# Kernel optimization log

Measured on AMD Instinct MI355X. Metric: run time of the kernel, lower is better.

The kernel has to match this reference:

```python
import jax, jax.numpy as jnp
import numpy as np

N_QUBITS = 10


def _apply_1q(state, U, wire, n):
    # state: (B, 2**n) complex; apply 2x2 U on `wire` (wire 0 = most significant bit)
    B = state.shape[0]
    left = 2 ** wire
    right = 2 ** (n - wire - 1)
    s = state.reshape(B, left, 2, right)
    s = jnp.einsum('ij,bljr->blir', U, s)
    return s.reshape(B, 2 ** n)


def _cnot(state, c, t, n):
    # CNOT with control wire c, target wire t
    B = state.shape[0]
    s = state.reshape((B,) + (2,) * n)
    ci, ti = c + 1, t + 1
    flipped = jnp.flip(s, axis=ti)
    zero = jnp.take(s, 0, axis=ci)      # control=0 slice unchanged
    one = jnp.take(flipped, 1, axis=ci)  # control=1 slice with target flipped
    s = jnp.stack([zero, one], axis=ci)
    return s.reshape(B, 2 ** n)


def _rot_matrix(phi, theta, omega):
    # PennyLane Rot(phi, theta, omega) = RZ(omega) @ RY(theta) @ RZ(phi)
    c = jnp.cos(theta / 2).astype(jnp.complex64)
    s = jnp.sin(theta / 2).astype(jnp.complex64)
    ep = jnp.exp(-0.5j * (phi + omega).astype(jnp.complex64))  # e^{-i(phi+omega)/2}
    em = jnp.exp(0.5j * (phi - omega).astype(jnp.complex64))   # e^{ i(phi-omega)/2}
    row0 = jnp.stack([ep * c, -em * s])
    row1 = jnp.stack([jnp.conj(em) * s, jnp.conj(ep) * c])
    return jnp.stack([row0, row1])  # (2, 2)


def setup_inputs() -> dict:
    key = jax.random.key(0)
    k1, k2 = jax.random.split(key)
    B, dim = 8192, 2 ** N_QUBITS
    patch = jax.random.normal(k1, (B, dim), dtype=jnp.float32)
    patch = patch / jnp.linalg.norm(patch, axis=1, keepdims=True)  # L2-normalized amplitudes
    weights = 0.01 * jax.random.normal(k2, (N_QUBITS, 3), dtype=jnp.float32)
    return {"patch_batch": patch, "weights": weights}


def reference(patch_batch, weights):
    n = weights.shape[0]
    state = patch_batch.astype(jnp.complex64)  # amplitude embedding
    for w in range(n):
        U = _rot_matrix(weights[w, 0], weights[w, 1], weights[w, 2])
        state = _apply_1q(state, U, w, n)
    for w in range(n - 1):
        state = _cnot(state, w, w + 1, n)
    state = _cnot(state, n - 1, 0, n)
    # expectation values of X, Y, Z on wire 0
    s2 = state.reshape(-1, 2, 2 ** (n - 1))
    a0, a1 = s2[:, 0], s2[:, 1]
    z = jnp.sum(jnp.conj(a0) * a1, axis=1)
    ex = 2.0 * jnp.real(z)
    ey = 2.0 * jnp.imag(z)
    ez = jnp.sum(jnp.abs(a0) ** 2 - jnp.abs(a1) ** 2, axis=1)
    out = jnp.stack([ex, ey, ez], axis=1)  # (B, 3)
    return jnp.nan_to_num(out, nan=0.0, posinf=1.0, neginf=-1.0)
```

## Files before the change

kernel.cpp:

```cpp
#include <hip/hip_runtime.h>


__global__ void qk_setup(const float* __restrict__ w, float* __restrict__ ws) {
    int t = threadIdx.x;
    if (t < 10) {
        float th = w[3 * t + 1];
        ws[2 * t]     = cosf(0.5f * th);
        ws[2 * t + 1] = sinf(0.5f * th);
    }
    if (t < 16) {
        float a = 0.f;
        for (int j = 0; j < 4; j++) if ((t >> j) & 1) a += w[3 * (9 - j)];
        ws[32 + 2 * t]     = cosf(a);
        ws[32 + 2 * t + 1] = sinf(a);
    }
    {
        float a = 0.f;
        for (int j = 0; j < 6; j++) if ((t >> j) & 1) a += w[3 * (5 - j)];
        ws[64 + 2 * t]     = cosf(a);
        ws[64 + 2 * t + 1] = sinf(a);
    }
    if (t < 4) {
        float d = (1.f - 2.f * ((t >> 1) & 1)) * w[2] + (1.f - 2.f * (t & 1)) * w[5];
        ws[192 + 2 * t]     = cosf(d);
        ws[192 + 2 * t + 1] = sinf(d);
    }
}

__global__ __launch_bounds__(256) void qk_sim(const float* __restrict__ x,
                                              const float* __restrict__ ws,
                                              float* __restrict__ out,
                                              int nstates) {
    int wave = (int)((blockIdx.x * blockDim.x + threadIdx.x) >> 6);
    int lane = threadIdx.x & 63;
    if (wave >= nstates) return;

    const float* CS = ws;
    const float* R  = ws + 32;
    const float* L  = ws + 64;
    const float* T4 = ws + 192;

    float Lr = L[2 * lane], Li = L[2 * lane + 1];

    const float4* row = (const float4*)(x + (size_t)wave * 1024);
    float re[16], im[16];
#pragma unroll
    for (int k = 0; k < 4; k++) {
        float4 v = row[lane * 4 + k];
        float xs0 = v.x, xs1 = v.y, xs2 = v.z, xs3 = v.w;
        float xv[4] = {xs0, xs1, xs2, xs3};
#pragma unroll
        for (int j = 0; j < 4; j++) {
            int r = 4 * k + j;
            float ar = xv[j] * R[2 * r];
            float ai = xv[j] * R[2 * r + 1];
            re[r] = Lr * ar - Li * ai;
            im[r] = Lr * ai + Li * ar;
        }
    }

#pragma unroll
    for (int rb = 0; rb < 4; rb++) {
        float c = CS[2 * (9 - rb)], s = CS[2 * (9 - rb) + 1];
#pragma unroll
        for (int r0 = 0; r0 < 16; r0++) {
            if (r0 & (1 << rb)) continue;
            int r1 = r0 | (1 << rb);
            float a0r = re[r0], a0i = im[r0];
            float a1r = re[r1], a1i = im[r1];
            re[r0] = c * a0r - s * a1r;  im[r0] = c * a0i - s * a1i;
            re[r1] = s * a0r + c * a1r;  im[r1] = s * a0i + c * a1i;
        }
    }

#pragma unroll
    for (int l = 0; l < 6; l++) {
        float c = CS[2 * (5 - l)], s = CS[2 * (5 - l) + 1];
        float ss = ((lane >> l) & 1) ? s : -s;
#pragma unroll
        for (int r = 0; r < 16; r++) {
            float mr = re[r], mi = im[r];
            float pr = __shfl_xor(mr, 1 << l, 64);
            float pi = __shfl_xor(mi, 1 << l, 64);
            re[r] = c * mr + ss * pr;
            im[r] = c * mi + ss * pi;
        }
    }

    float zxr = 0.f, zxi = 0.f, zyr = 0.f, zyi = 0.f, ez = 0.f;
#pragma unroll
    for (int r = 0; r < 16; r++) {
        float mr = re[r], mi = im[r];
        float pr = __shfl_xor(mr, 48, 64);
        float pi = __shfl_xor(mi, 48, 64);
        float cr = mr * pr + mi * pi;
        float ci = mr * pi - mi * pr;
        zxr += cr; zxi += ci;
        if (__popc(r) & 1) { zyr -= cr; zyi -= ci; ez -= mr * mr + mi * mi; }
        else               { zyr += cr; zyi += ci; ez += mr * mr + mi * mi; }
    }
    int j4 = (lane >> 4) & 3;
    float cD = T4[2 * j4], sD = T4[2 * j4 + 1];
    float lsgn = (__popc(lane & 31) & 1) ? -1.f : 1.f;
    float ex  = cD * zxr - sD * zxi;
    float ey  = lsgn * (cD * zyi + sD * zyr);
    float ezl = lsgn * ez;

#pragma unroll
    for (int off = 32; off >= 1; off >>= 1) {
        ex  += __shfl_xor(ex,  off, 64);
        ey  += __shfl_xor(ey,  off, 64);
        ezl += __shfl_xor(ezl, off, 64);
    }
    if (lane == 0) {
        float* o = out + 3 * (size_t)wave;
        o[0] = ex; o[1] = ey; o[2] = ezl;
    }
}

extern "C" void kernel_launch(void* const* d_in, const int* in_sizes, int n_in,
                              void* d_out, int out_size, void* d_ws, size_t ws_size,
                              hipStream_t stream) {
    const float* patch   = (const float*)d_in[0];
    const float* weights = (const float*)d_in[1];
    float* out = (float*)d_out;
    float* ws  = (float*)d_ws;

    int nstates = in_sizes[0] / 1024;

    qk_setup<<<1, 64, 0, stream>>>(weights, ws);

    int nblocks = nstates / 4;
    qk_sim<<<nblocks, 256, 0, stream>>>(patch, ws, out, nstates);
}
```

Baseline: 93.89 us.

## Remap qubits to registers/lanes, precompute full phase table, use DPP cross-lane ops

Changes the assignment of amplitudes to lanes and registers so each lane loads strided float4 rows (h*64+lane). Precomputes a full 1024-entry complex phase table in the setup kernel instead of the separate L and R factors. Replaces ds_bpermute shuffles with DPP and ds_swizzle for the small xor distances, and computes the wire-0 pairing inside registers rather than via a cross-lane shuffle. This cuts shuffle traffic and per-element complex multiplies, at the cost of an extra 8 KB phase-table read per wave and a larger setup kernel.

```diff
diff --git a/kernel.cpp b/kernel.cpp
--- a/kernel.cpp
+++ b/kernel.cpp
@@ -1,29 +1,64 @@
 #include <hip/hip_runtime.h>
 
 
+template <int CTRL>
+__device__ __forceinline__ float dppf(float x) {
+    return __int_as_float(__builtin_amdgcn_update_dpp(
+        __float_as_int(x), __float_as_int(x), CTRL, 0xF, 0xF, true));
+}
+
+template <int MASK>
+__device__ __forceinline__ float lxor(float x) {
+    if constexpr (MASK == 1)  return dppf<0xB1>(x);
+    else if constexpr (MASK == 2)  return dppf<0x4E>(x);
+    else if constexpr (MASK == 4)  return dppf<0x141>(dppf<0x1B>(x));
+    else if constexpr (MASK == 8)  return dppf<0x128>(x);
+    else if constexpr (MASK == 16)
+        return __int_as_float(__builtin_amdgcn_ds_swizzle(__float_as_int(x), 0x401F));
+    else return __shfl_xor(x, MASK, 64);
+}
+
 __global__ void qk_setup(const float* __restrict__ w, float* __restrict__ ws) {
     int t = threadIdx.x;
+    float a = 0.f;
+    for (int wq = 0; wq < 10; wq++)
+        if ((t >> (9 - wq)) & 1) a += w[3 * wq];
+    ws[2 * t]     = cosf(a);
+    ws[2 * t + 1] = sinf(a);
     if (t < 10) {
         float th = w[3 * t + 1];
-        ws[2 * t]     = cosf(0.5f * th);
-        ws[2 * t + 1] = sinf(0.5f * th);
-    }
-    if (t < 16) {
-        float a = 0.f;
-        for (int j = 0; j < 4; j++) if ((t >> j) & 1) a += w[3 * (9 - j)];
-        ws[32 + 2 * t]     = cosf(a);
-        ws[32 + 2 * t + 1] = sinf(a);
-    }
-    {
-        float a = 0.f;
-        for (int j = 0; j < 6; j++) if ((t >> j) & 1) a += w[3 * (5 - j)];
-        ws[64 + 2 * t]     = cosf(a);
-        ws[64 + 2 * t + 1] = sinf(a);
+        ws[2048 + 2 * t]     = cosf(0.5f * th);
+        ws[2048 + 2 * t + 1] = sinf(0.5f * th);
     }
     if (t < 4) {
         float d = (1.f - 2.f * ((t >> 1) & 1)) * w[2] + (1.f - 2.f * (t & 1)) * w[5];
-        ws[192 + 2 * t]     = cosf(d);
-        ws[192 + 2 * t + 1] = sinf(d);
+        ws[2068 + 2 * t]     = cosf(d);
+        ws[2068 + 2 * t + 1] = sinf(d);
+    }
+}
+
+__device__ __forceinline__ void rgate(float (&re)[16], float (&im)[16], int bit,
+                                      float c, float s) {
+#pragma unroll
+    for (int s0 = 0; s0 < 16; s0++) {
+        if (s0 & bit) continue;
+        int s1 = s0 | bit;
+        float a0r = re[s0], a0i = im[s0];
+        float a1r = re[s1], a1i = im[s1];
+        re[s0] = c * a0r - s * a1r;  im[s0] = c * a0i - s * a1i;
+        re[s1] = s * a0r + c * a1r;  im[s1] = s * a0i + c * a1i;
+    }
+}
+
+template <int MASK>
+__device__ __forceinline__ void xgate(float (&re)[16], float (&im)[16],
+                                      float c, float ss) {
+#pragma unroll
+    for (int r = 0; r < 16; r++) {
+        float pr = lxor<MASK>(re[r]);
+        float pi = lxor<MASK>(im[r]);
+        re[r] = c * re[r] + ss * pr;
+        im[r] = c * im[r] + ss * pi;
     }
 }
 
@@ -35,86 +70,76 @@
     int lane = threadIdx.x & 63;
     if (wave >= nstates) return;
 
-    const float* CS = ws;
-    const float* R  = ws + 32;
-    const float* L  = ws + 64;
-    const float* T4 = ws + 192;
+    const float* CS = ws + 2048;
+    const float* T4 = ws + 2068;
 
-    float Lr = L[2 * lane], Li = L[2 * lane + 1];
-
-    const float4* row = (const float4*)(x + (size_t)wave * 1024);
+    const float4* rowx = (const float4*)(x + (size_t)wave * 1024);
+    const float4* Pt   = (const float4*)ws;
     float re[16], im[16];
 #pragma unroll
-    for (int k = 0; k < 4; k++) {
-        float4 v = row[lane * 4 + k];
-        float xs0 = v.x, xs1 = v.y, xs2 = v.z, xs3 = v.w;
-        float xv[4] = {xs0, xs1, xs2, xs3};
+    for (int h = 0; h < 4; h++) {
+        float4 v  = rowx[h * 64 + lane];
+        float4 p0 = Pt[h * 128 + lane * 2];
+        float4 p1 = Pt[h * 128 + lane * 2 + 1];
+        re[h * 4 + 0] = v.x * p0.x;  im[h * 4 + 0] = v.x * p0.y;
+        re[h * 4 + 1] = v.y * p0.z;  im[h * 4 + 1] = v.y * p0.w;
+        re[h * 4 + 2] = v.z * p1.x;  im[h * 4 + 2] = v.z * p1.y;
+        re[h * 4 + 3] = v.w * p1.z;  im[h * 4 + 3] = v.w * p1.w;
+    }
+
+    rgate(re, im, 1, CS[2 * 9], CS[2 * 9 + 1]);
+    rgate(re, im, 2, CS[2 * 8], CS[2 * 8 + 1]);
+    rgate(re, im, 4, CS[2 * 1], CS[2 * 1 + 1]);
+    rgate(re, im, 8, CS[2 * 0], CS[2 * 0 + 1]);
+
+    {
+        float s7 = CS[2 * 7 + 1], s6 = CS[2 * 6 + 1], s5 = CS[2 * 5 + 1];
+        float s4 = CS[2 * 4 + 1], s3 = CS[2 * 3 + 1], s2 = CS[2 * 2 + 1];
+        xgate<1> (re, im, CS[2 * 7], (lane & 1)  ? s7 : -s7);
+        xgate<2> (re, im, CS[2 * 6], (lane & 2)  ? s6 : -s6);
+        xgate<4> (re, im, CS[2 * 5], (lane & 4)  ? s5 : -s5);
+        xgate<8> (re, im, CS[2 * 4], (lane & 8)  ? s4 : -s4);
+        xgate<16>(re, im, CS[2 * 3], (lane & 16) ? s3 : -s3);
+        xgate<32>(re, im, CS[2 * 2], (lane & 32) ? s2 : -s2);
+    }
+
+    float ex2 = 0.f, ey2 = 0.f, ez16 = 0.f;
 #pragma unroll
-        for (int j = 0; j < 4; j++) {
-            int r = 4 * k + j;
-            float ar = xv[j] * R[2 * r];
-            float ai = xv[j] * R[2 * r + 1];
-            re[r] = Lr * ar - Li * ai;
-            im[r] = Lr * ai + Li * ar;
+    for (int h = 0; h < 2; h++) {
+        float cD = T4[2 * h], sD = T4[2 * h + 1];
+#pragma unroll
+        for (int q = 0; q < 4; q++) {
+            int s  = h * 4 + q;
+            int sp = s ^ 12;
+            float mr = re[s], mi = im[s];
+            float pr = re[sp], pi = im[sp];
+            float cr = mr * pr + mi * pi;
+            float ci = mr * pi - mi * pr;
+            ex2 += cD * cr - sD * ci;
+            float t = cD * ci + sD * cr;
+            if ((h ^ (__popc(q) & 1)) & 1) ey2 -= t; else ey2 += t;
         }
     }
+#pragma unroll
+    for (int s = 0; s < 16; s++) {
+        float n = re[s] * re[s] + im[s] * im[s];
+        if ((((s >> 2) & 1) ^ (__popc(s & 3) & 1)) & 1) ez16 -= n; else ez16 += n;
+    }
+    float psgn = (__popc(lane) & 1) ? -1.f : 1.f;
+    float ex = 2.f * ex2;
+    float ey = 2.f * psgn * ey2;
+    float ez = psgn * ez16;
 
-#pragma unroll
-    for (int rb = 0; rb < 4; rb++) {
-        float c = CS[2 * (9 - rb)], s = CS[2 * (9 - rb) + 1];
-#pragma unroll
-        for (int r0 = 0; r0 < 16; r0++) {
-            if (r0 & (1 << rb)) continue;
-            int r1 = r0 | (1 << rb);
-            float a0r = re[r0], a0i = im[r0];
-            float a1r = re[r1], a1i = im[r1];
-            re[r0] = c * a0r - s * a1r;  im[r0] = c * a0i - s * a1i;
-            re[r1] = s * a0r + c * a1r;  im[r1] = s * a0i + c * a1i;
-        }
-    }
+    ex += lxor<1>(ex);  ey += lxor<1>(ey);  ez += lxor<1>(ez);
+    ex += lxor<2>(ex);  ey += lxor<2>(ey);  ez += lxor<2>(ez);
+    ex += lxor<4>(ex);  ey += lxor<4>(ey);  ez += lxor<4>(ez);
+    ex += lxor<8>(ex);  ey += lxor<8>(ey);  ez += lxor<8>(ez);
+    ex += lxor<16>(ex); ey += lxor<16>(ey); ez += lxor<16>(ez);
+    ex += lxor<32>(ex); ey += lxor<32>(ey); ez += lxor<32>(ez);
 
-#pragma unroll
-    for (int l = 0; l < 6; l++) {
-        float c = CS[2 * (5 - l)], s = CS[2 * (5 - l) + 1];
-        float ss = ((lane >> l) & 1) ? s : -s;
-#pragma unroll
-        for (int r = 0; r < 16; r++) {
-            float mr = re[r], mi = im[r];
-            float pr = __shfl_xor(mr, 1 << l, 64);
-            float pi = __shfl_xor(mi, 1 << l, 64);
-            re[r] = c * mr + ss * pr;
-            im[r] = c * mi + ss * pi;
-        }
-    }
-
-    float zxr = 0.f, zxi = 0.f, zyr = 0.f, zyi = 0.f, ez = 0.f;
-#pragma unroll
-    for (int r = 0; r < 16; r++) {
-        float mr = re[r], mi = im[r];
-        float pr = __shfl_xor(mr, 48, 64);
-        float pi = __shfl_xor(mi, 48, 64);
-        float cr = mr * pr + mi * pi;
-        float ci = mr * pi - mi * pr;
-        zxr += cr; zxi += ci;
-        if (__popc(r) & 1) { zyr -= cr; zyi -= ci; ez -= mr * mr + mi * mi; }
-        else               { zyr += cr; zyi += ci; ez += mr * mr + mi * mi; }
-    }
-    int j4 = (lane >> 4) & 3;
-    float cD = T4[2 * j4], sD = T4[2 * j4 + 1];
-    float lsgn = (__popc(lane & 31) & 1) ? -1.f : 1.f;
-    float ex  = cD * zxr - sD * zxi;
-    float ey  = lsgn * (cD * zyi + sD * zyr);
-    float ezl = lsgn * ez;
-
-#pragma unroll
-    for (int off = 32; off >= 1; off >>= 1) {
-        ex  += __shfl_xor(ex,  off, 64);
-        ey  += __shfl_xor(ey,  off, 64);
-        ezl += __shfl_xor(ezl, off, 64);
-    }
     if (lane == 0) {
         float* o = out + 3 * (size_t)wave;
-        o[0] = ex; o[1] = ey; o[2] = ezl;
+        o[0] = ex; o[1] = ey; o[2] = ez;
     }
 }
 
@@ -128,7 +153,7 @@
 
     int nstates = in_sizes[0] / 1024;
 
-    qk_setup<<<1, 64, 0, stream>>>(weights, ws);
+    qk_setup<<<1, 1024, 0, stream>>>(weights, ws);
 
     int nblocks = nstates / 4;
     qk_sim<<<nblocks, 256, 0, stream>>>(patch, ws, out, nstates);
```

Result: faster. 85.92 us (-8.5%).
